# Performance work log

Hardware: AMD Instinct MI355X
Metric: run time of the kernel (lower is better)

Reference implementation:

```python
import jax, jax.numpy as jnp
import numpy as np

B, S, E, H = 4, 2048, 1024, 16
DK = E // H  # 64


def setup_inputs() -> dict:
    key = jax.random.key(0)
    ks = jax.random.split(key, 11)
    s_in = 1.0 / np.sqrt(E)
    return {
        "query": jax.random.normal(ks[0], (B, S, E), jnp.float32),
        "key_": jax.random.normal(ks[1], (B, S, E), jnp.float32),
        "value": jax.random.normal(ks[2], (B, S, E), jnp.float32),
        # nn.Linear weights stored as [out, in]; applied as x @ W.T + b
        "Wq": jax.random.uniform(ks[3], (E, E), jnp.float32, -s_in, s_in),
        "bq": jax.random.uniform(ks[4], (E,), jnp.float32, -s_in, s_in),
        "Wk": jax.random.uniform(ks[5], (E, E), jnp.float32, -s_in, s_in),
        "bk": jax.random.uniform(ks[6], (E,), jnp.float32, -s_in, s_in),
        "Wv": jax.random.uniform(ks[7], (E, E), jnp.float32, -s_in, s_in),
        "bv": jax.random.uniform(ks[8], (E,), jnp.float32, -s_in, s_in),
        "Wo": jax.random.uniform(ks[9], (E, E), jnp.float32, -s_in, s_in),
        "bo": jax.random.uniform(ks[10], (E,), jnp.float32, -s_in, s_in),
    }


def reference(query, key_, value, Wq, bq, Wk, bk, Wv, bv, Wo, bo):
    scale = 1.0 / np.sqrt(DK).astype(np.float32)
    Q = query @ Wq.T + bq   # [B,S,E]
    K = key_ @ Wk.T + bk
    V = value @ Wv.T + bv
    # split heads: [B,S,H,DK] (slicing dim -1 into contiguous per-head chunks)
    Qh = Q.reshape(B, S, H, DK)
    Kh = K.reshape(B, S, H, DK)
    Vh = V.reshape(B, S, H, DK)
    scores = jnp.einsum('bqhd,bkhd->bhqk', Qh, Kh) * scale  # [B,H,S,S]
    probs = jax.nn.softmax(scores, axis=-1)
    ctx = jnp.einsum('bhqk,bkhd->bqhd', probs, Vh).reshape(B, S, E)
    out = ctx @ Wo.T + bo
    return out
```

## Files before the change

kernel.cpp:

```cpp
#include <hip/hip_runtime.h>
#include <stdint.h>
#include <stddef.h>

constexpr int BB = 4, SS = 2048, EE = 1024, HH = 16, DKH = 64;
constexpr int MM = BB * SS;
constexpr float SM_SCALE_LOG2 = 0.18033688011112042f;

typedef unsigned short u16;
typedef __attribute__((ext_vector_type(8))) short bf16x8;
typedef __attribute__((ext_vector_type(8))) unsigned short u16x8;
typedef __attribute__((ext_vector_type(4))) float f32x4;
typedef __attribute__((ext_vector_type(16))) float f32x16;
typedef __attribute__((ext_vector_type(2))) unsigned int u32x2;
typedef __attribute__((ext_vector_type(4))) unsigned int u32x4;

__device__ __forceinline__ u16 f2bf(float f) {
  unsigned u = __builtin_bit_cast(unsigned, f);
  u += 0x7FFFu + ((u >> 16) & 1u);
  return (u16)(u >> 16);
}

__device__ __forceinline__ unsigned pack2(float lo, float hi) {
  unsigned r;
  asm("v_cvt_pk_bf16_f32 %0, %1, %2" : "=v"(r) : "v"(lo), "v"(hi));
  return r;
}

__device__ __forceinline__ void gld16(const void* g, void* l) {
  __builtin_amdgcn_global_load_lds(
      (const __attribute__((address_space(1))) unsigned int*)g,
      (__attribute__((address_space(3))) unsigned int*)l, 16, 0, 0);
}

struct Cvt4 { const float* in[4]; u16* out[4]; };

__global__ void cvt_bf16_x4(Cvt4 p, int n8) {
  int i = blockIdx.x * 256 + threadIdx.x;
  if (i >= n8) return;
  const int z = blockIdx.y;
  const float4* src = (const float4*)p.in[z] + (size_t)i * 2;
  float4 a = src[0], b = src[1];
  u16x8 v;
  v[0] = f2bf(a.x); v[1] = f2bf(a.y); v[2] = f2bf(a.z); v[3] = f2bf(a.w);
  v[4] = f2bf(b.x); v[5] = f2bf(b.y); v[6] = f2bf(b.z); v[7] = f2bf(b.w);
  *((u16x8*)p.out[z] + i) = v;
}

struct GemmPtrs {
  const u16* A[3];
  const float* A32[3];
  const u16* W[3];
  const float* bias[3];
  void* C[3];
  float scale[3];
  int mode[3];
};

template <int AF32>
__global__ __launch_bounds__(256, 3) void gemm32(GemmPtrs p, int M, int N, int K) {
  extern __shared__ __align__(16) char smem[];
  float* SAf = (float*)smem;
  u16* SAb = (u16*)smem;
  u16* SB = (u16*)(smem + (AF32 ? 32768 : 16384));
  const int t = threadIdx.x, l = t & 63, w = t >> 6;
  const int lq = l & 31, hi = l >> 5;
  const int wm = w >> 1, wn = w & 1;
  const int z = blockIdx.z;
  const u16* Ab = p.A[z];
  const float* Af = p.A32[z];
  const u16* W = p.W[z];
  const float* bias = p.bias[z];

  const int nwg = gridDim.x * gridDim.y;
  const int o = blockIdx.y * gridDim.x + blockIdx.x;
  const int sw = (o & 7) * (nwg >> 3) + (o >> 3);
  const int n0 = (sw % gridDim.x) * 128;
  const int m0 = (sw / gridDim.x) * 128;

  f32x16 acc[2][2];
#pragma unroll
  for (int i = 0; i < 2; ++i)
#pragma unroll
    for (int j = 0; j < 2; ++j)
#pragma unroll
      for (int r = 0; r < 16; ++r) acc[i][j][r] = 0.f;

  auto stage = [&](int buf, int kt) {
    if (AF32) {
#pragma unroll
      for (int i = 0; i < 4; ++i) {
        const int ci = i * 256 + t;
        const int r = ci >> 3, P = ci & 7;
        const int L = P ^ (r & 7);
        gld16(Af + (size_t)(m0 + r) * K + kt * 32 + L * 4,
              (char*)(SAf + buf * 128 * 32) + (i * 256 + (t & ~63)) * 16);
      }
    } else {
#pragma unroll
      for (int i = 0; i < 2; ++i) {
        const int ci = i * 256 + t;
        const int r = ci >> 3, P = ci & 7;
        const int L = P ^ (r & 7);
        const int m = r + ((L & 4) << 4);
        const int kc = L & 3;
        gld16(Ab + (size_t)(m0 + m) * K + kt * 32 + kc * 8,
              (char*)(SAb + buf * 64 * 64) + (i * 256 + (t & ~63)) * 16);
      }
    }
#pragma unroll
    for (int i = 0; i < 2; ++i) {
      const int ci = i * 256 + t;
      const int r = ci >> 3, P = ci & 7;
      const int L = P ^ (r & 7);
      const int m = r + ((L & 4) << 4);
      const int kc = L & 3;
      gld16(W + (size_t)(n0 + m) * K + kt * 32 + kc * 8,
            (char*)(SB + buf * 64 * 64) + (i * 256 + (t & ~63)) * 16);
    }
  };

  stage(0, 0);
  __syncthreads();
  int cur = 0;
  const int NT = K >> 5;
  const int lsw = lq & 7;
  for (int kt = 0; kt < NT; ++kt) {
    if (kt + 1 < NT) stage(cur ^ 1, kt + 1);

    bf16x8 a0[2], a1[2], b0[2], b1[2];
    if (AF32) {
      const float* Ac = SAf + cur * 128 * 32;
#pragma unroll
      for (int ks = 0; ks < 2; ++ks) {
#pragma unroll
        for (int fi = 0; fi < 2; ++fi) {
          const int R = wm * 64 + fi * 32 + lq;
          const char* rowp = (const char*)(Ac + (size_t)R * 32);
          const int L0 = 4 * ks + 2 * hi;
          const f32x4 v0 = *(const f32x4*)(rowp + ((L0 ^ (R & 7)) * 16));
          const f32x4 v1 = *(const f32x4*)(rowp + (((L0 + 1) ^ (R & 7)) * 16));
          u32x4 pk;
          pk[0] = pack2(v0[0], v0[1]);
          pk[1] = pack2(v0[2], v0[3]);
          pk[2] = pack2(v1[0], v1[1]);
          pk[3] = pack2(v1[2], v1[3]);
          const bf16x8 af = __builtin_bit_cast(bf16x8, pk);
          if (fi == 0) a0[ks] = af;
          else a1[ks] = af;
        }
      }
    } else {
      const u16* Ac = SAb + cur * 64 * 64;
#pragma unroll
      for (int ks = 0; ks < 2; ++ks) {
        const int ca = ((wm << 2) + (ks << 1) + hi) ^ lsw;
        a0[ks] = *(const bf16x8*)(Ac + lq * 64 + ca * 8);
        a1[ks] = *(const bf16x8*)(Ac + (32 + lq) * 64 + ca * 8);
      }
    }
    {
      const u16* Bc = SB + cur * 64 * 64;
#pragma unroll
      for (int ks = 0; ks < 2; ++ks) {
        const int cb = ((wn << 2) + (ks << 1) + hi) ^ lsw;
        b0[ks] = *(const bf16x8*)(Bc + lq * 64 + cb * 8);
        b1[ks] = *(const bf16x8*)(Bc + (32 + lq) * 64 + cb * 8);
      }
    }

    __builtin_amdgcn_s_setprio(1);
#pragma unroll
    for (int ks = 0; ks < 2; ++ks) {
      acc[0][0] = __builtin_amdgcn_mfma_f32_32x32x16_bf16(a0[ks], b0[ks], acc[0][0], 0, 0, 0);
      acc[0][1] = __builtin_amdgcn_mfma_f32_32x32x16_bf16(a0[ks], b1[ks], acc[0][1], 0, 0, 0);
      acc[1][0] = __builtin_amdgcn_mfma_f32_32x32x16_bf16(a1[ks], b0[ks], acc[1][0], 0, 0, 0);
      acc[1][1] = __builtin_amdgcn_mfma_f32_32x32x16_bf16(a1[ks], b1[ks], acc[1][1], 0, 0, 0);
    }
    __builtin_amdgcn_s_setprio(0);
    __syncthreads();
    cur ^= 1;
  }

  const float sc = p.scale[z];
  const int mode = p.mode[z];
#pragma unroll
  for (int fr = 0; fr < 2; ++fr) {
#pragma unroll
    for (int fc = 0; fc < 2; ++fc) {
      const int col = n0 + wn * 64 + fc * 32 + lq;
      const float bv = bias[col];
#pragma unroll
      for (int g = 0; g < 4; ++g) {
        const int mb = m0 + wm * 64 + fr * 32 + 8 * g + 4 * hi;
        float v[4];
#pragma unroll
        for (int j = 0; j < 4; ++j) v[j] = (acc[fr][fc][4 * g + j] + bv) * sc;
        if (mode == 1) {
#pragma unroll
          for (int j = 0; j < 4; ++j)
            ((float*)p.C[z])[(size_t)(mb + j) * N + col] = v[j];
        } else if (mode == 0) {
#pragma unroll
          for (int j = 0; j < 4; ++j)
            ((u16*)p.C[z])[(size_t)(mb + j) * N + col] = f2bf(v[j]);
        } else {
          const int b = mb >> 11, s = mb & 2047;
          u16* dst = (u16*)p.C[z] +
                     ((size_t)((b * 16 + (col >> 6)) * 64 + (col & 63))) * SS + s;
          uint2 pk;
          pk.x = pack2(v[0], v[1]);
          pk.y = pack2(v[2], v[3]);
          *(uint2*)dst = pk;
        }
      }
    }
  }
}

__global__ __launch_bounds__(256, 4) void attn_fwd3(const u16* __restrict__ Q,
                                                    const u16* __restrict__ K,
                                                    const u16* __restrict__ Vt,
                                                    u16* __restrict__ C) {
  __shared__ __align__(16) u16 Ks[2][64 * 64];
  __shared__ __align__(16) u16 Vs[2][64 * 64];

  const int t = threadIdx.x, l = t & 63, w = t >> 6;
  const int lq = l & 31, hi = l >> 5;
  const int q0 = blockIdx.x * 128;
  const int bh = blockIdx.y, bb = bh >> 4, hh = bh & 15;

  const u16* qp = Q + ((size_t)(bb * SS + q0 + w * 32 + lq)) * EE + hh * 64 + hi * 8;
  bf16x8 qf[4];
  qf[0] = *(const bf16x8*)(qp);
  qf[1] = *(const bf16x8*)(qp + 16);
  qf[2] = *(const bf16x8*)(qp + 32);
  qf[3] = *(const bf16x8*)(qp + 48);

  const u16* Kbase = K + (size_t)bb * SS * EE + hh * 64;
  const u16* Vbase = Vt + (size_t)bh * DKH * SS;

  f32x16 accA, accB;
  f32x16 z16;
#pragma unroll
  for (int i = 0; i < 16; ++i) { accA[i] = 0.f; accB[i] = 0.f; z16[i] = 0.f; }
  float lsum = 0.0f;

  auto stage = [&](int buf, int kt) {
#pragma unroll
    for (int i = 0; i < 2; ++i) {
      const int slot = i * 256 + t;
      const int row = slot >> 3, pc = slot & 7;
      const int lc = pc ^ (row & 7);
      const int lbyte = (i * 256 + (t & ~63)) * 16;
      gld16(Kbase + (size_t)(kt * 64 + row) * EE + lc * 8, (char*)&Ks[buf][0] + lbyte);
      gld16(Vbase + (size_t)row * SS + kt * 64 + lc * 8, (char*)&Vs[buf][0] + lbyte);
    }
  };

  auto mkfrag = [&](const f32x16& p, int base) -> bf16x8 {
    unsigned A0 = pack2(p[base + 0], p[base + 1]);
    unsigned A1 = pack2(p[base + 2], p[base + 3]);
    unsigned B0 = pack2(p[base + 4], p[base + 5]);
    unsigned B1 = pack2(p[base + 6], p[base + 7]);
    u32x2 r0 = __builtin_amdgcn_permlane32_swap(A0, B0, false, false);
    u32x2 r1 = __builtin_amdgcn_permlane32_swap(A1, B1, false, false);
    u32x4 fr;
    fr[0] = r0[0]; fr[1] = r1[0]; fr[2] = r0[1]; fr[3] = r1[1];
    return __builtin_bit_cast(bf16x8, fr);
  };

  stage(0, 0);
  __syncthreads();
  int cur = 0;
  for (int kt = 0; kt < SS / 64; ++kt) {
    if (kt + 1 < SS / 64) stage(cur ^ 1, kt + 1);
    const u16* Kc = &Ks[cur][0];
    const u16* Vc = &Vs[cur][0];

    f32x16 s0, s1;
    __builtin_amdgcn_s_setprio(1);
    {
      const int c = hi ^ (lq & 7);
      bf16x8 kf0 = *(const bf16x8*)(Kc + lq * 64 + c * 8);
      bf16x8 kf1 = *(const bf16x8*)(Kc + (32 + lq) * 64 + c * 8);
      s0 = __builtin_amdgcn_mfma_f32_32x32x16_bf16(kf0, qf[0], z16, 0, 0, 0);
      s1 = __builtin_amdgcn_mfma_f32_32x32x16_bf16(kf1, qf[0], z16, 0, 0, 0);
    }
#pragma unroll
    for (int m = 1; m < 4; ++m) {
      const int c = (2 * m + hi) ^ (lq & 7);
      bf16x8 kf0 = *(const bf16x8*)(Kc + lq * 64 + c * 8);
      bf16x8 kf1 = *(const bf16x8*)(Kc + (32 + lq) * 64 + c * 8);
      s0 = __builtin_amdgcn_mfma_f32_32x32x16_bf16(kf0, qf[m], s0, 0, 0, 0);
      s1 = __builtin_amdgcn_mfma_f32_32x32x16_bf16(kf1, qf[m], s1, 0, 0, 0);
    }
    __builtin_amdgcn_s_setprio(0);

#pragma unroll
    for (int i = 0; i < 16; ++i) {
      s0[i] = __builtin_amdgcn_exp2f(s0[i]);
      s1[i] = __builtin_amdgcn_exp2f(s1[i]);
    }
    float sa = 0.f, sb = 0.f, sc2 = 0.f, sd = 0.f;
#pragma unroll
    for (int i = 0; i < 8; ++i) {
      sa += s0[i]; sb += s0[i + 8];
      sc2 += s1[i]; sd += s1[i + 8];
    }
    lsum += (sa + sb) + (sc2 + sd);

    bf16x8 pf[4];
    pf[0] = mkfrag(s0, 0);
    pf[1] = mkfrag(s0, 8);
    pf[2] = mkfrag(s1, 0);
    pf[3] = mkfrag(s1, 8);

    __builtin_amdgcn_s_setprio(1);
#pragma unroll
    for (int s = 0; s < 4; ++s) {
      const int c = (2 * s + hi) ^ (lq & 7);
      bf16x8 vf0 = *(const bf16x8*)(Vc + lq * 64 + c * 8);
      bf16x8 vf1 = *(const bf16x8*)(Vc + (32 + lq) * 64 + c * 8);
      accA = __builtin_amdgcn_mfma_f32_32x32x16_bf16(vf0, pf[s], accA, 0, 0, 0);
      accB = __builtin_amdgcn_mfma_f32_32x32x16_bf16(vf1, pf[s], accB, 0, 0, 0);
    }
    __builtin_amdgcn_s_setprio(0);
    __syncthreads();
    cur ^= 1;
  }

  const float inv = 1.0f / (lsum + __shfl_xor(lsum, 32));
  char* Tw = (char*)&Ks[0][0] + w * 4096;
#pragma unroll
  for (int g = 0; g < 4; ++g) {
    uint2 pa, pb;
    pa.x = pack2(accA[4 * g + 0] * inv, accA[4 * g + 1] * inv);
    pa.y = pack2(accA[4 * g + 2] * inv, accA[4 * g + 3] * inv);
    pb.x = pack2(accB[4 * g + 0] * inv, accB[4 * g + 1] * inv);
    pb.y = pack2(accB[4 * g + 2] * inv, accB[4 * g + 3] * inv);
    const int sub = 8 * hi, sw = (lq & 7) << 4;
    *(uint2*)(Tw + lq * 128 + (((g) << 4) ^ sw) + sub) = pa;
    *(uint2*)(Tw + lq * 128 + (((4 + g) << 4) ^ sw) + sub) = pb;
  }
  const int qr0 = l >> 3, ch = l & 7;
#pragma unroll
  for (int ps = 0; ps < 4; ++ps) {
    const int qr = ps * 8 + qr0;
    u32x4 vv = *(const u32x4*)(Tw + qr * 128 + ((ch ^ (qr & 7)) << 4));
    u16* dst = C + ((size_t)(bb * SS + q0 + w * 32 + qr)) * EE + hh * 64 + ch * 8;
    *(u32x4*)dst = vv;
  }
}

extern "C" void kernel_launch(void* const* d_in, const int* in_sizes, int n_in,
                              void* d_out, int out_size, void* d_ws, size_t ws_size,
                              hipStream_t stream) {
  (void)in_sizes; (void)n_in; (void)out_size; (void)ws_size;
  const float* query = (const float*)d_in[0];
  const float* key_  = (const float*)d_in[1];
  const float* value = (const float*)d_in[2];
  const float* Wq = (const float*)d_in[3];
  const float* bq = (const float*)d_in[4];
  const float* Wk = (const float*)d_in[5];
  const float* bk = (const float*)d_in[6];
  const float* Wv = (const float*)d_in[7];
  const float* bv = (const float*)d_in[8];
  const float* Wo = (const float*)d_in[9];
  const float* bo = (const float*)d_in[10];

  char* ws = (char*)d_ws;
  const size_t SZX = (size_t)MM * EE * 2;
  const size_t SZW = (size_t)EE * EE * 2;
  u16* Qb  = (u16*)(ws + 0 * SZX);
  u16* Kb  = (u16*)(ws + 1 * SZX);
  u16* Vtb = (u16*)(ws + 2 * SZX);
  u16* Cb  = (u16*)(ws + 3 * SZX);
  u16* Wqb = (u16*)(ws + 4 * SZX + 0 * SZW);
  u16* Wkb = (u16*)(ws + 4 * SZX + 1 * SZW);
  u16* Wvb = (u16*)(ws + 4 * SZX + 2 * SZW);
  u16* Wob = (u16*)(ws + 4 * SZX + 3 * SZW);

  const int n8w = EE * EE / 8;

  Cvt4 cw{};
  cw.in[0] = Wq; cw.in[1] = Wk; cw.in[2] = Wv; cw.in[3] = Wo;
  cw.out[0] = Wqb; cw.out[1] = Wkb; cw.out[2] = Wvb; cw.out[3] = Wob;
  cvt_bf16_x4<<<dim3(n8w / 256, 4), 256, 0, stream>>>(cw, n8w);

  GemmPtrs g{};
  g.A32[0] = query; g.A32[1] = key_; g.A32[2] = value;
  g.W[0] = Wqb; g.W[1] = Wkb; g.W[2] = Wvb;
  g.bias[0] = bq; g.bias[1] = bk; g.bias[2] = bv;
  g.C[0] = Qb; g.C[1] = Kb; g.C[2] = Vtb;
  g.scale[0] = SM_SCALE_LOG2; g.scale[1] = 1.0f; g.scale[2] = 1.0f;
  g.mode[0] = 0; g.mode[1] = 0; g.mode[2] = 2;
  gemm32<1><<<dim3(EE / 128, MM / 128, 3), 256, 49152, stream>>>(g, MM, EE, EE);

  attn_fwd3<<<dim3(SS / 128, BB * HH), 256, 0, stream>>>(Qb, Kb, Vtb, Cb);

  GemmPtrs g2{};
  g2.A[0] = Cb; g2.W[0] = Wob; g2.bias[0] = bo; g2.C[0] = d_out;
  g2.scale[0] = 1.0f; g2.mode[0] = 1;
  gemm32<0><<<dim3(EE / 128, MM / 128, 1), 256, 32768, stream>>>(g2, MM, EE, EE);
}
```

Measured before the change: 197.7 us.

## Convert fp32 activations to bf16 at LDS write time in QKV GEMM

Adds a dedicated QKV projection kernel that loads fp32 activations into registers two tiles ahead, converts them to bf16, and writes them into a bf16 LDS buffer. Previously the fp32 tile was staged directly into LDS and converted on every fragment read. The change halves the A-tile LDS footprint (32 KB total, launch bounds raised to 4 blocks) and stops each wave from repeating the conversion. In exchange the global loads go through registers instead of direct-to-LDS, which raises register pressure and puts the load latency into the software pipeline.

New measurement: 295.1 us. 1.49x slower.

```diff
diff --git a/kernel.cpp b/kernel.cpp
--- a/kernel.cpp
+++ b/kernel.cpp
@@ -56,131 +56,10 @@
   int mode[3];
 };
 
-template <int AF32>
-__global__ __launch_bounds__(256, 3) void gemm32(GemmPtrs p, int M, int N, int K) {
-  extern __shared__ __align__(16) char smem[];
-  float* SAf = (float*)smem;
-  u16* SAb = (u16*)smem;
-  u16* SB = (u16*)(smem + (AF32 ? 32768 : 16384));
-  const int t = threadIdx.x, l = t & 63, w = t >> 6;
-  const int lq = l & 31, hi = l >> 5;
-  const int wm = w >> 1, wn = w & 1;
-  const int z = blockIdx.z;
-  const u16* Ab = p.A[z];
-  const float* Af = p.A32[z];
-  const u16* W = p.W[z];
-  const float* bias = p.bias[z];
-
-  const int nwg = gridDim.x * gridDim.y;
-  const int o = blockIdx.y * gridDim.x + blockIdx.x;
-  const int sw = (o & 7) * (nwg >> 3) + (o >> 3);
-  const int n0 = (sw % gridDim.x) * 128;
-  const int m0 = (sw / gridDim.x) * 128;
-
-  f32x16 acc[2][2];
-#pragma unroll
-  for (int i = 0; i < 2; ++i)
-#pragma unroll
-    for (int j = 0; j < 2; ++j)
-#pragma unroll
-      for (int r = 0; r < 16; ++r) acc[i][j][r] = 0.f;
-
-  auto stage = [&](int buf, int kt) {
-    if (AF32) {
-#pragma unroll
-      for (int i = 0; i < 4; ++i) {
-        const int ci = i * 256 + t;
-        const int r = ci >> 3, P = ci & 7;
-        const int L = P ^ (r & 7);
-        gld16(Af + (size_t)(m0 + r) * K + kt * 32 + L * 4,
-              (char*)(SAf + buf * 128 * 32) + (i * 256 + (t & ~63)) * 16);
-      }
-    } else {
-#pragma unroll
-      for (int i = 0; i < 2; ++i) {
-        const int ci = i * 256 + t;
-        const int r = ci >> 3, P = ci & 7;
-        const int L = P ^ (r & 7);
-        const int m = r + ((L & 4) << 4);
-        const int kc = L & 3;
-        gld16(Ab + (size_t)(m0 + m) * K + kt * 32 + kc * 8,
-              (char*)(SAb + buf * 64 * 64) + (i * 256 + (t & ~63)) * 16);
-      }
-    }
-#pragma unroll
-    for (int i = 0; i < 2; ++i) {
-      const int ci = i * 256 + t;
-      const int r = ci >> 3, P = ci & 7;
-      const int L = P ^ (r & 7);
-      const int m = r + ((L & 4) << 4);
-      const int kc = L & 3;
-      gld16(W + (size_t)(n0 + m) * K + kt * 32 + kc * 8,
-            (char*)(SB + buf * 64 * 64) + (i * 256 + (t & ~63)) * 16);
-    }
-  };
-
-  stage(0, 0);
-  __syncthreads();
-  int cur = 0;
-  const int NT = K >> 5;
-  const int lsw = lq & 7;
-  for (int kt = 0; kt < NT; ++kt) {
-    if (kt + 1 < NT) stage(cur ^ 1, kt + 1);
-
-    bf16x8 a0[2], a1[2], b0[2], b1[2];
-    if (AF32) {
-      const float* Ac = SAf + cur * 128 * 32;
-#pragma unroll
-      for (int ks = 0; ks < 2; ++ks) {
-#pragma unroll
-        for (int fi = 0; fi < 2; ++fi) {
-          const int R = wm * 64 + fi * 32 + lq;
-          const char* rowp = (const char*)(Ac + (size_t)R * 32);
-          const int L0 = 4 * ks + 2 * hi;
-          const f32x4 v0 = *(const f32x4*)(rowp + ((L0 ^ (R & 7)) * 16));
-          const f32x4 v1 = *(const f32x4*)(rowp + (((L0 + 1) ^ (R & 7)) * 16));
-          u32x4 pk;
-          pk[0] = pack2(v0[0], v0[1]);
-          pk[1] = pack2(v0[2], v0[3]);
-          pk[2] = pack2(v1[0], v1[1]);
-          pk[3] = pack2(v1[2], v1[3]);
-          const bf16x8 af = __builtin_bit_cast(bf16x8, pk);
-          if (fi == 0) a0[ks] = af;
-          else a1[ks] = af;
-        }
-      }
-    } else {
-      const u16* Ac = SAb + cur * 64 * 64;
-#pragma unroll
-      for (int ks = 0; ks < 2; ++ks) {
-        const int ca = ((wm << 2) + (ks << 1) + hi) ^ lsw;
-        a0[ks] = *(const bf16x8*)(Ac + lq * 64 + ca * 8);
-        a1[ks] = *(const bf16x8*)(Ac + (32 + lq) * 64 + ca * 8);
-      }
-    }
-    {
-      const u16* Bc = SB + cur * 64 * 64;
-#pragma unroll
-      for (int ks = 0; ks < 2; ++ks) {
-        const int cb = ((wn << 2) + (ks << 1) + hi) ^ lsw;
-        b0[ks] = *(const bf16x8*)(Bc + lq * 64 + cb * 8);
-        b1[ks] = *(const bf16x8*)(Bc + (32 + lq) * 64 + cb * 8);
-      }
-    }
-
-    __builtin_amdgcn_s_setprio(1);
-#pragma unroll
-    for (int ks = 0; ks < 2; ++ks) {
-      acc[0][0] = __builtin_amdgcn_mfma_f32_32x32x16_bf16(a0[ks], b0[ks], acc[0][0], 0, 0, 0);
-      acc[0][1] = __builtin_amdgcn_mfma_f32_32x32x16_bf16(a0[ks], b1[ks], acc[0][1], 0, 0, 0);
-      acc[1][0] = __builtin_amdgcn_mfma_f32_32x32x16_bf16(a1[ks], b0[ks], acc[1][0], 0, 0, 0);
-      acc[1][1] = __builtin_amdgcn_mfma_f32_32x32x16_bf16(a1[ks], b1[ks], acc[1][1], 0, 0, 0);
-    }
-    __builtin_amdgcn_s_setprio(0);
-    __syncthreads();
-    cur ^= 1;
-  }
-
+template <typename ACC>
+__device__ __forceinline__ void store_c(const GemmPtrs& p, int z, int N,
+                                        const ACC& acc, int m0, int n0, int wm,
+                                        int wn, int lq, int hi) {
   const float sc = p.scale[z];
   const int mode = p.mode[z];
 #pragma unroll
@@ -188,7 +67,7 @@
 #pragma unroll
     for (int fc = 0; fc < 2; ++fc) {
       const int col = n0 + wn * 64 + fc * 32 + lq;
-      const float bv = bias[col];
+      const float bv = p.bias[z][col];
 #pragma unroll
       for (int g = 0; g < 4; ++g) {
         const int mb = m0 + wm * 64 + fr * 32 + 8 * g + 4 * hi;
@@ -215,6 +94,198 @@
       }
     }
   }
+}
+
+__global__ __launch_bounds__(256, 4) void gemm32f(GemmPtrs p, int M, int N, int K) {
+  __shared__ __align__(16) u16 SA[2][64 * 64];
+  __shared__ __align__(16) u16 SB[2][64 * 64];
+  const int t = threadIdx.x, l = t & 63, w = t >> 6;
+  const int lq = l & 31, hi = l >> 5;
+  const int wm = w >> 1, wn = w & 1;
+  const int z = blockIdx.z;
+  const float* Af = p.A32[z];
+  const u16* W = p.W[z];
+
+  const int nwg = gridDim.x * gridDim.y;
+  const int o = blockIdx.y * gridDim.x + blockIdx.x;
+  const int sw = (o & 7) * (nwg >> 3) + (o >> 3);
+  const int n0 = (sw % gridDim.x) * 128;
+  const int m0 = (sw / gridDim.x) * 128;
+
+  f32x16 acc[2][2];
+#pragma unroll
+  for (int i = 0; i < 2; ++i)
+#pragma unroll
+    for (int j = 0; j < 2; ++j)
+#pragma unroll
+      for (int r = 0; r < 16; ++r) acc[i][j][r] = 0.f;
+
+  auto stageB = [&](int buf, int kt) {
+#pragma unroll
+    for (int i = 0; i < 2; ++i) {
+      const int ci = i * 256 + t;
+      const int r = ci >> 3, P = ci & 7;
+      const int L = P ^ (r & 7);
+      const int m = r + ((L & 4) << 4);
+      const int kc = L & 3;
+      gld16(W + (size_t)(n0 + m) * K + kt * 32 + kc * 8,
+            (char*)&SB[buf][0] + (i * 256 + (t & ~63)) * 16);
+    }
+  };
+  auto loadAf = [&](int kt, float4 (&rg)[2][2]) {
+#pragma unroll
+    for (int i = 0; i < 2; ++i) {
+      const int ci = i * 256 + t;
+      const int r = ci >> 3, P = ci & 7;
+      const int L = P ^ (r & 7);
+      const int m = r + ((L & 4) << 4);
+      const int kc = L & 3;
+      const float4* src = (const float4*)(Af + (size_t)(m0 + m) * K + kt * 32 + kc * 8);
+      rg[i][0] = src[0];
+      rg[i][1] = src[1];
+    }
+  };
+  auto writeAf = [&](int buf, float4 (&rg)[2][2]) {
+#pragma unroll
+    for (int i = 0; i < 2; ++i) {
+      const int ci = i * 256 + t;
+      u32x4 pk;
+      pk[0] = pack2(rg[i][0].x, rg[i][0].y);
+      pk[1] = pack2(rg[i][0].z, rg[i][0].w);
+      pk[2] = pack2(rg[i][1].x, rg[i][1].y);
+      pk[3] = pack2(rg[i][1].z, rg[i][1].w);
+      *(u32x4*)((char*)&SA[buf][0] + ci * 16) = pk;
+    }
+  };
+
+  const int NT = K >> 5;
+  const int lsw = lq & 7;
+  float4 avA[2][2], avB[2][2];
+
+  loadAf(0, avA);
+  writeAf(0, avA);
+  loadAf(1, avB);
+  stageB(0, 0);
+  __syncthreads();
+
+  auto body = [&](int kt, float4 (&Wr)[2][2], float4 (&Lr)[2][2]) {
+    if (kt + 1 < NT) stageB((kt + 1) & 1, kt + 1);
+    if (kt + 2 < NT) loadAf(kt + 2, Lr);
+    const u16* Ac = &SA[kt & 1][0];
+    const u16* Bc = &SB[kt & 1][0];
+    bf16x8 a0[2], a1[2], b0[2], b1[2];
+#pragma unroll
+    for (int ks = 0; ks < 2; ++ks) {
+      const int ca = ((wm << 2) + (ks << 1) + hi) ^ lsw;
+      const int cb = ((wn << 2) + (ks << 1) + hi) ^ lsw;
+      a0[ks] = *(const bf16x8*)(Ac + lq * 64 + ca * 8);
+      a1[ks] = *(const bf16x8*)(Ac + (32 + lq) * 64 + ca * 8);
+      b0[ks] = *(const bf16x8*)(Bc + lq * 64 + cb * 8);
+      b1[ks] = *(const bf16x8*)(Bc + (32 + lq) * 64 + cb * 8);
+    }
+    __builtin_amdgcn_s_setprio(1);
+#pragma unroll
+    for (int ks = 0; ks < 2; ++ks) {
+      acc[0][0] = __builtin_amdgcn_mfma_f32_32x32x16_bf16(a0[ks], b0[ks], acc[0][0], 0, 0, 0);
+      acc[0][1] = __builtin_amdgcn_mfma_f32_32x32x16_bf16(a0[ks], b1[ks], acc[0][1], 0, 0, 0);
+      acc[1][0] = __builtin_amdgcn_mfma_f32_32x32x16_bf16(a1[ks], b0[ks], acc[1][0], 0, 0, 0);
+      acc[1][1] = __builtin_amdgcn_mfma_f32_32x32x16_bf16(a1[ks], b1[ks], acc[1][1], 0, 0, 0);
+    }
+    __builtin_amdgcn_s_setprio(0);
+    if (kt + 1 < NT) writeAf((kt + 1) & 1, Wr);
+    __syncthreads();
+  };
+
+  for (int kt = 0; kt < NT; kt += 2) {
+    body(kt, avB, avA);
+    body(kt + 1, avA, avB);
+  }
+
+  store_c(p, z, N, acc, m0, n0, wm, wn, lq, hi);
+}
+
+template <int AF32>
+__global__ __launch_bounds__(256, 3) void gemm32(GemmPtrs p, int M, int N, int K) {
+  extern __shared__ __align__(16) char smem[];
+  u16* SAb = (u16*)smem;
+  u16* SB = (u16*)(smem + 16384);
+  const int t = threadIdx.x, l = t & 63, w = t >> 6;
+  const int lq = l & 31, hi = l >> 5;
+  const int wm = w >> 1, wn = w & 1;
+  const int z = blockIdx.z;
+  const u16* Ab = p.A[z];
+  const u16* W = p.W[z];
+
+  const int nwg = gridDim.x * gridDim.y;
+  const int o = blockIdx.y * gridDim.x + blockIdx.x;
+  const int sw = (o & 7) * (nwg >> 3) + (o >> 3);
+  const int n0 = (sw % gridDim.x) * 128;
+  const int m0 = (sw / gridDim.x) * 128;
+
+  f32x16 acc[2][2];
+#pragma unroll
+  for (int i = 0; i < 2; ++i)
+#pragma unroll
+    for (int j = 0; j < 2; ++j)
+#pragma unroll
+      for (int r = 0; r < 16; ++r) acc[i][j][r] = 0.f;
+
+  auto stage = [&](int buf, int kt) {
+#pragma unroll
+    for (int i = 0; i < 2; ++i) {
+      const int ci = i * 256 + t;
+      const int r = ci >> 3, P = ci & 7;
+      const int L = P ^ (r & 7);
+      const int m = r + ((L & 4) << 4);
+      const int kc = L & 3;
+      gld16(Ab + (size_t)(m0 + m) * K + kt * 32 + kc * 8,
+            (char*)(SAb + buf * 64 * 64) + (i * 256 + (t & ~63)) * 16);
+    }
+#pragma unroll
+    for (int i = 0; i < 2; ++i) {
+      const int ci = i * 256 + t;
+      const int r = ci >> 3, P = ci & 7;
+      const int L = P ^ (r & 7);
+      const int m = r + ((L & 4) << 4);
+      const int kc = L & 3;
+      gld16(W + (size_t)(n0 + m) * K + kt * 32 + kc * 8,
+            (char*)(SB + buf * 64 * 64) + (i * 256 + (t & ~63)) * 16);
+    }
+  };
+
+  stage(0, 0);
+  __syncthreads();
+  int cur = 0;
+  const int NT = K >> 5;
+  const int lsw = lq & 7;
+  for (int kt = 0; kt < NT; ++kt) {
+    if (kt + 1 < NT) stage(cur ^ 1, kt + 1);
+    const u16* Ac = SAb + cur * 64 * 64;
+    const u16* Bc = SB + cur * 64 * 64;
+    bf16x8 a0[2], a1[2], b0[2], b1[2];
+#pragma unroll
+    for (int ks = 0; ks < 2; ++ks) {
+      const int ca = ((wm << 2) + (ks << 1) + hi) ^ lsw;
+      const int cb = ((wn << 2) + (ks << 1) + hi) ^ lsw;
+      a0[ks] = *(const bf16x8*)(Ac + lq * 64 + ca * 8);
+      a1[ks] = *(const bf16x8*)(Ac + (32 + lq) * 64 + ca * 8);
+      b0[ks] = *(const bf16x8*)(Bc + lq * 64 + cb * 8);
+      b1[ks] = *(const bf16x8*)(Bc + (32 + lq) * 64 + cb * 8);
+    }
+    __builtin_amdgcn_s_setprio(1);
+#pragma unroll
+    for (int ks = 0; ks < 2; ++ks) {
+      acc[0][0] = __builtin_amdgcn_mfma_f32_32x32x16_bf16(a0[ks], b0[ks], acc[0][0], 0, 0, 0);
+      acc[0][1] = __builtin_amdgcn_mfma_f32_32x32x16_bf16(a0[ks], b1[ks], acc[0][1], 0, 0, 0);
+      acc[1][0] = __builtin_amdgcn_mfma_f32_32x32x16_bf16(a1[ks], b0[ks], acc[1][0], 0, 0, 0);
+      acc[1][1] = __builtin_amdgcn_mfma_f32_32x32x16_bf16(a1[ks], b1[ks], acc[1][1], 0, 0, 0);
+    }
+    __builtin_amdgcn_s_setprio(0);
+    __syncthreads();
+    cur ^= 1;
+  }
+
+  store_c(p, z, N, acc, m0, n0, wm, wn, lq, hi);
 }
 
 __global__ __launch_bounds__(256, 4) void attn_fwd3(const u16* __restrict__ Q,
@@ -394,7 +465,7 @@
   g.C[0] = Qb; g.C[1] = Kb; g.C[2] = Vtb;
   g.scale[0] = SM_SCALE_LOG2; g.scale[1] = 1.0f; g.scale[2] = 1.0f;
   g.mode[0] = 0; g.mode[1] = 0; g.mode[2] = 2;
-  gemm32<1><<<dim3(EE / 128, MM / 128, 3), 256, 49152, stream>>>(g, MM, EE, EE);
+  gemm32f<<<dim3(EE / 128, MM / 128, 3), 256, 0, stream>>>(g, MM, EE, EE);
 
   attn_fwd3<<<dim3(SS / 128, BB * HH), 256, 0, stream>>>(Qb, Kb, Vtb, Cb);
 
```
